# Optimization experiments

Measured on AMD Instinct MI355X. Metric: run time of the kernel, lower is better.

Reference implementation:

```python
import jax, jax.numpy as jnp
import numpy as np
import itertools

GRID_NUM = 12
VOXEL_SIZE = 0.12
OFFSET = GRID_NUM * VOXEL_SIZE / 2.0  # 0.72
G3 = GRID_NUM ** 3


def setup_inputs() -> dict:
    key = jax.random.key(0)
    k0, k1, k2, k3 = jax.random.split(key, 4)
    B, L0, L1, C = 4, 2048, 1024, 64
    x0 = jax.random.normal(k0, (B, L0, C), dtype=jnp.float32)
    x1 = jax.random.normal(k1, (B, L1, C), dtype=jnp.float32)
    # positions in [-0.3, 0.3) so delta_pos + OFFSET lies inside the grid [0, 1.44)
    pos0 = (jax.random.uniform(k2, (B, L0, 3), dtype=jnp.float32) - 0.5) * 0.6
    pos1 = (jax.random.uniform(k3, (B, L1, 3), dtype=jnp.float32) - 0.5) * 0.6
    return {"x0": x0, "x1": x1, "pos0": pos0, "pos1": pos1}


def _p2g_trilinear(pos, prob, seg, num_seg):
    """Trilinear point-to-grid splat.
    pos: (N,3) continuous coords in grid units' metric space; prob: (N,); seg: (N,) int segment id.
    Returns (num_seg, G3)."""
    c = pos / VOXEL_SIZE - 0.5          # voxel-center coordinates
    base = jnp.floor(c)
    frac = c - base                      # (N,3) in [0,1)
    base = base.astype(jnp.int32)
    out = jnp.zeros((num_seg * G3,), dtype=prob.dtype)
    for corner in itertools.product((0, 1), repeat=3):
        idx = base + jnp.asarray(corner, dtype=jnp.int32)  # (N,3)
        w = prob
        for d in range(3):
            w = w * (frac[:, d] if corner[d] else (1.0 - frac[:, d]))
        valid = jnp.all((idx >= 0) & (idx < GRID_NUM), axis=-1)
        flat = seg * G3 + idx[:, 0] * (GRID_NUM * GRID_NUM) + idx[:, 1] * GRID_NUM + idx[:, 2]
        flat = jnp.where(valid, flat, 0)
        out = out.at[flat].add(jnp.where(valid, w, 0.0))
    return out.reshape(num_seg, G3)


def reference(x0, x1, pos0, pos1):
    B, L0, C = x0.shape
    L1 = x1.shape[1]
    # scaled correlation + row softmax (stable; max-subtraction is math-identical)
    corr = jnp.einsum('blc,bmc->blm', x0, x1) / jnp.sqrt(jnp.asarray(C, x0.dtype))
    prob = jax.nn.softmax(corr, axis=-1)                       # (B,L0,L1)
    correspondence = jnp.einsum('blm,bmc->blc', prob, pos1)    # (B,L0,3)
    flow = correspondence - pos0
    # point-to-grid distribution of match probability over relative offsets
    delta = pos1[:, None, :, :] - pos0[:, :, None, :]          # (B,L0,L1,3)
    pos_f = delta.reshape(-1, 3) + OFFSET
    prob_f = prob.reshape(-1)
    N = B * L0 * L1
    seg = jnp.arange(N, dtype=jnp.int32) // L1                 # (N,) query-point segment id
    grid = _p2g_trilinear(pos_f, prob_f, seg, B * L0)          # (B*L0, G3)
    probs_grid = grid.reshape(B, L0, G3)
    return (flow, probs_grid)
```

## Files before the change

### kernel.cpp

```cpp
#include <hip/hip_runtime.h>
#include <stdint.h>

#define GRID_NUM 12
#define G3 1728
#define L0V 2048
#define L1V 1024
#define CV 64
#define RT 16

typedef __attribute__((ext_vector_type(8))) short short8;
typedef __attribute__((ext_vector_type(4))) short short4v;
typedef __attribute__((ext_vector_type(4))) float f32x4;

__device__ __forceinline__ unsigned short f2bf(float f) {
    union { float f; unsigned u; } v; v.f = f;
    unsigned u = v.u;
    u += 0x7fffu + ((u >> 16) & 1u);
    return (unsigned short)(u >> 16);
}
__device__ __forceinline__ float bf2f(unsigned short h) {
    union { unsigned u; float f; } v; v.u = ((unsigned)h) << 16;
    return v.f;
}

__device__ __forceinline__ void gload16(const void* g, void* l) {
    __builtin_amdgcn_global_load_lds(
        (const __attribute__((address_space(1))) unsigned int*)(uintptr_t)g,
        (__attribute__((address_space(3))) unsigned int*)(uintptr_t)l,
        16, 0, 0);
}

__global__ __launch_bounds__(256) void cvt_x1_kernel(
    const float* __restrict__ x1, unsigned short* __restrict__ ximg)
{
    const int g  = blockIdx.x * 256 + threadIdx.x;
    const int kg = g >> 3;
    const int j8 = g & 7;
    const int key = kg & 1023;
    const int ch  = key >> 6;
    const int kk  = key & 63;
    const int bi  = kg >> 10;

    const float4* src = (const float4*)(x1 + (size_t)kg * CV + j8 * 8);
    const float4 v0 = src[0], v1 = src[1];
    const float vv[8] = {v0.x, v0.y, v0.z, v0.w, v1.x, v1.y, v1.z, v1.w};
    short8 hi, lo;
    #pragma unroll
    for (int i = 0; i < 8; ++i) {
        const unsigned short h = f2bf(vv[i]);
        hi[i] = (short)h;
        lo[i] = (short)f2bf(vv[i] - bf2f(h));
    }
    char* base = (char*)ximg + ((size_t)(bi * 16 + ch)) * 16384;
    const int off = kk * 128 + ((j8 * 16) ^ ((kk & 7) << 4));
    *(short8*)(base + off) = hi;
    *(short8*)(base + 8192 + off) = lo;
}

__global__ __launch_bounds__(256) void cvt_pos_kernel(
    const float* __restrict__ pos1, float4* __restrict__ pos1p, int n)
{
    const int k = blockIdx.x * 256 + threadIdx.x;
    if (k < n) {
        float4 v;
        v.x = pos1[k * 3 + 0];
        v.y = pos1[k * 3 + 1];
        v.z = pos1[k * 3 + 2];
        v.w = 0.f;
        pos1p[k] = v;
    }
}

__global__ __launch_bounds__(256) void corr_probs_kernel(
    const float* __restrict__ x0, const unsigned short* __restrict__ ximg,
    const float* __restrict__ pos0, const float* __restrict__ pos1,
    float* __restrict__ out_flow, unsigned short* __restrict__ probs_bf,
    float* __restrict__ rscale)
{
    const int r0 = blockIdx.x * RT;
    const int b  = r0 >> 11;
    const int t  = threadIdx.x;
    const int lane = t & 63;
    const int w    = t >> 6;
    const int l15  = lane & 15;
    const int q    = lane >> 4;

    __shared__ __align__(16) short sX0h[RT * 64], sX0l[RT * 64];
    __shared__ __align__(16) char  sX1[2][16384];
    __shared__ __align__(16) float sp1[L1V * 3];
    __shared__ float sred[4][RT][4];

    {
        const int row = t >> 4;
        const float4 v = ((const float4*)(x0 + (size_t)(r0 + row) * CV))[t & 15];
        const unsigned short h0 = f2bf(v.x), h1 = f2bf(v.y), h2 = f2bf(v.z), h3 = f2bf(v.w);
        const short4v hi = { (short)h0, (short)h1, (short)h2, (short)h3 };
        const short4v lo = { (short)f2bf(v.x - bf2f(h0)), (short)f2bf(v.y - bf2f(h1)),
                             (short)f2bf(v.z - bf2f(h2)), (short)f2bf(v.w - bf2f(h3)) };
        const int off = row * 128 + (((t & 15) * 8) ^ ((row & 7) << 4));
        *(short4v*)((char*)sX0h + off) = hi;
        *(short4v*)((char*)sX0l + off) = lo;
    }
    {
        const float4* ps = (const float4*)(pos1 + (size_t)b * L1V * 3);
        #pragma unroll
        for (int i = 0; i < 3; ++i)
            ((float4*)sp1)[i * 256 + t] = ps[i * 256 + t];
    }

    const char* img = (const char*)ximg + (size_t)b * (16 * 16384);
    #pragma unroll
    for (int i = 0; i < 4; ++i)
        gload16(img + (w * 4 + i) * 1024 + lane * 16,
                sX1[0] + (w * 4 + i) * 1024);
    __syncthreads();

    const int ma    = w * 16 + l15;
    const int abase = ma * 128;
    const int asw   = (ma & 7) << 4;
    const int bbase = l15 * 128;
    const int bsw   = (l15 & 7) << 4;

    const int ka0 = (q * 8) * 2, ka1 = (32 + q * 8) * 2;
    const short8 bh0 = *(const short8*)((const char*)sX0h + bbase + (ka0 ^ bsw));
    const short8 bh1 = *(const short8*)((const char*)sX0h + bbase + (ka1 ^ bsw));
    const short8 bl0 = *(const short8*)((const char*)sX0l + bbase + (ka0 ^ bsw));
    const short8 bl1 = *(const short8*)((const char*)sX0l + bbase + (ka1 ^ bsw));

    float s_a = 0.f, cx_a = 0.f, cy_a = 0.f, cz_a = 0.f;

    for (int ch = 0; ch < 16; ++ch) {
        const int buf = ch & 1;
        if (ch < 15) {
            const char* s = img + (ch + 1) * 16384;
            char* d = sX1[buf ^ 1];
            #pragma unroll
            for (int i = 0; i < 4; ++i)
                gload16(s + (w * 4 + i) * 1024 + lane * 16, d + (w * 4 + i) * 1024);
            asm volatile("s_waitcnt vmcnt(4)" ::: "memory");
        } else {
            asm volatile("s_waitcnt vmcnt(1)" ::: "memory");
        }
        __builtin_amdgcn_s_barrier();

        const char* Xh = sX1[buf];
        const char* Xl = Xh + 8192;
        f32x4 acc = {0.f, 0.f, 0.f, 0.f};
        {
            const short8 ah0 = *(const short8*)(Xh + abase + (ka0 ^ asw));
            const short8 al0 = *(const short8*)(Xl + abase + (ka0 ^ asw));
            const short8 ah1 = *(const short8*)(Xh + abase + (ka1 ^ asw));
            const short8 al1 = *(const short8*)(Xl + abase + (ka1 ^ asw));
            acc = __builtin_amdgcn_mfma_f32_16x16x32_bf16(ah0, bh0, acc, 0, 0, 0);
            acc = __builtin_amdgcn_mfma_f32_16x16x32_bf16(ah0, bl0, acc, 0, 0, 0);
            acc = __builtin_amdgcn_mfma_f32_16x16x32_bf16(al0, bh0, acc, 0, 0, 0);
            acc = __builtin_amdgcn_mfma_f32_16x16x32_bf16(ah1, bh1, acc, 0, 0, 0);
            acc = __builtin_amdgcn_mfma_f32_16x16x32_bf16(ah1, bl1, acc, 0, 0, 0);
            acc = __builtin_amdgcn_mfma_f32_16x16x32_bf16(al1, bh1, acc, 0, 0, 0);
        }

        unsigned short eb[4];
        #pragma unroll
        for (int rg = 0; rg < 4; ++rg) {
            const int kc = ch * 64 + w * 16 + q * 4 + rg;
            const float e = __expf(acc[rg] * 0.125f);
            eb[rg] = f2bf(e);
            s_a += e;
            cx_a = fmaf(e, sp1[kc * 3 + 0], cx_a);
            cy_a = fmaf(e, sp1[kc * 3 + 1], cy_a);
            cz_a = fmaf(e, sp1[kc * 3 + 2], cz_a);
        }
        const short4v ev = { (short)eb[0], (short)eb[1], (short)eb[2], (short)eb[3] };
        *(short4v*)(probs_bf + (size_t)(r0 + l15) * L1V + ch * 64 + w * 16 + q * 4) = ev;

        __builtin_amdgcn_s_barrier();
    }

    s_a  += __shfl_xor(s_a, 16, 64);  s_a  += __shfl_xor(s_a, 32, 64);
    cx_a += __shfl_xor(cx_a, 16, 64); cx_a += __shfl_xor(cx_a, 32, 64);
    cy_a += __shfl_xor(cy_a, 16, 64); cy_a += __shfl_xor(cy_a, 32, 64);
    cz_a += __shfl_xor(cz_a, 16, 64); cz_a += __shfl_xor(cz_a, 32, 64);
    if (lane < 16) {
        sred[w][l15][0] = s_a;  sred[w][l15][1] = cx_a;
        sred[w][l15][2] = cy_a; sred[w][l15][3] = cz_a;
    }
    __syncthreads();

    if (t < RT) {
        const float S  = (sred[0][t][0] + sred[1][t][0]) + (sred[2][t][0] + sred[3][t][0]);
        const float CX = (sred[0][t][1] + sred[1][t][1]) + (sred[2][t][1] + sred[3][t][1]);
        const float CY = (sred[0][t][2] + sred[1][t][2]) + (sred[2][t][2] + sred[3][t][2]);
        const float CZ = (sred[0][t][3] + sred[1][t][3]) + (sred[2][t][3] + sred[3][t][3]);
        const float rs = 1.0f / S;
        rscale[r0 + t] = rs;
        out_flow[(r0 + t) * 3 + 0] = CX * rs - pos0[(r0 + t) * 3 + 0];
        out_flow[(r0 + t) * 3 + 1] = CY * rs - pos0[(r0 + t) * 3 + 1];
        out_flow[(r0 + t) * 3 + 2] = CZ * rs - pos0[(r0 + t) * 3 + 2];
    }
}

__global__ __launch_bounds__(256, 4) void splat_mfma_kernel(
    const unsigned short* __restrict__ probs_bf, const float* __restrict__ rscale,
    const float* __restrict__ pos0, const float4* __restrict__ pos1p,
    float* __restrict__ out_grid)
{
    const int t    = threadIdx.x;
    const int lane = t & 63;
    const int w    = t >> 6;
    const int r    = blockIdx.x * 4 + w;
    const int b    = r >> 11;

    __shared__ __align__(16) short sAll[4][4608];
    char* sR = (char*)sAll[w];
    char* sZ = (char*)sAll[w] + 8192;

    const float inv = 1.0f / 0.12f;
    const float p0x = pos0[r * 3 + 0];
    const float p0y = pos0[r * 3 + 1];
    const float p0z = pos0[r * 3 + 2];
    const float4* p1p = pos1p + (size_t)b * L1V;
    const unsigned short* prow = probs_bf + (size_t)r * L1V;

    const int mnx = (int)floorf((-0.3f - p0x + 0.72f) * inv - 0.5f);
    const int mny = (int)floorf((-0.3f - p0y + 0.72f) * inv - 0.5f);
    const int mnz = (int)floorf((-0.3f - p0z + 0.72f) * inv - 0.5f);

    {
        const short8 z8 = {0, 0, 0, 0, 0, 0, 0, 0};
        #pragma unroll
        for (int j = 0; j < 9; ++j)
            *(short8*)(sR + lane * 16 + j * 1024) = z8;
    }

    const int l15  = lane & 15;
    const int q16  = (lane >> 4) * 16;
    const int asw  = (l15 & 7) << 4;
    const int aoff0 = l15 * 128 + ((0  + q16) ^ asw);
    const int aoff1 = l15 * 128 + ((64 + q16) ^ asw);
    const int zrow = l15 & 7;
    const int bsw  = zrow << 4;
    const int boff0 = zrow * 128 + ((0  + q16) ^ bsw);
    const int boff1 = zrow * 128 + ((64 + q16) ^ bsw);
    const int lane2 = lane * 2;

    f32x4 acc[4];
    #pragma unroll
    for (int mt = 0; mt < 4; ++mt) acc[mt] = (f32x4){0.f, 0.f, 0.f, 0.f};

    char *P0 = sR + lane2, *P1 = sR + lane2, *P2 = sR + lane2,
         *P3 = sR + lane2, *P4 = sZ + lane2, *P5 = sZ + lane2;

    float4 pc = p1p[lane];
    float pv  = bf2f(prow[lane]);

    asm volatile("s_waitcnt lgkmcnt(0)" ::: "memory");

    for (int ch = 0; ch < 16; ++ch) {
        float4 nc = pc;
        float  nv = pv;
        if (ch < 15) {
            const int nk = (ch + 1) * 64 + lane;
            nc = p1p[nk];
            nv = bf2f(prow[nk]);
        }

        const float ax = ((pc.x - p0x) + 0.72f) * inv - 0.5f;
        const float ay = ((pc.y - p0y) + 0.72f) * inv - 0.5f;
        const float az = ((pc.z - p0z) + 0.72f) * inv - 0.5f;
        const float fxf = floorf(ax), fyf = floorf(ay), fzf = floorf(az);
        const float fx = ax - fxf, fy = ay - fyf, fz = az - fzf;
        const int rix = (int)fxf - mnx;
        const int riy = (int)fyf - mny;
        const int riz = (int)fzf - mnz;
        const float wx0 = 1.f - fx, wy0 = 1.f - fy, wz0 = 1.f - fz;
        const float a0p = pv * wx0, a1p = pv * fx;
        const unsigned short r00 = f2bf(a0p * wy0), r01 = f2bf(a0p * fy);
        const unsigned short r10 = f2bf(a1p * wy0), r11 = f2bf(a1p * fy);
        const unsigned short z0 = f2bf(wz0), z1 = f2bf(fz);

        const int c00 = rix * 8 + riy;
        char* A0 = sR + (c00    ) * 128 + (lane2 ^ (((c00    ) & 7) << 4));
        char* A1 = sR + (c00 + 1) * 128 + (lane2 ^ (((c00 + 1) & 7) << 4));
        char* A2 = sR + (c00 + 8) * 128 + (lane2 ^ (((c00 + 8) & 7) << 4));
        char* A3 = sR + (c00 + 9) * 128 + (lane2 ^ (((c00 + 9) & 7) << 4));
        char* Z0a = sZ + riz * 128 + (lane2 ^ (riz << 4));
        char* Z1a = sZ + (riz + 1) * 128 + (lane2 ^ ((riz + 1) << 4));

        *(short*)P0 = 0; *(short*)P1 = 0; *(short*)P2 = 0;
        *(short*)P3 = 0; *(short*)P4 = 0; *(short*)P5 = 0;
        *(short*)A0 = (short)r00; *(short*)A1 = (short)r01;
        *(short*)A2 = (short)r10; *(short*)A3 = (short)r11;
        *(short*)Z0a = (short)z0; *(short*)Z1a = (short)z1;

        const short8 b0 = *(const short8*)(sZ + boff0);
        const short8 b1 = *(const short8*)(sZ + boff1);
        #pragma unroll
        for (int mt = 0; mt < 4; ++mt) {
            const short8 a0 = *(const short8*)(sR + mt * 2048 + aoff0);
            const short8 a1 = *(const short8*)(sR + mt * 2048 + aoff1);
            acc[mt] = __builtin_amdgcn_mfma_f32_16x16x32_bf16(a0, b0, acc[mt], 0, 0, 0);
            acc[mt] = __builtin_amdgcn_mfma_f32_16x16x32_bf16(a1, b1, acc[mt], 0, 0, 0);
        }

        P0 = A0; P1 = A1; P2 = A2; P3 = A3; P4 = Z0a; P5 = Z1a;
        pc = nc; pv = nv;
    }

    const float rs = rscale[r];
    float* og = out_grid + (size_t)r * G3;
    {
        const float4 z4 = {0.f, 0.f, 0.f, 0.f};
        float4* og4 = (float4*)og;
        #pragma unroll
        for (int j = 0; j < 6; ++j) og4[j * 64 + lane] = z4;
        if (lane < 48) og4[384 + lane] = z4;
    }
    asm volatile("s_waitcnt vmcnt(0)" ::: "memory");

    const int zB = lane & 15;
    if (zB < 8) {
        const int gz = mnz + zB;
        if (gz <= 11) {
            const int h4 = (lane >> 4) * 4;
            const int rxm = 11 - mnx;
            const int rym = 11 - mny;
            float* base2 = og + mnx * 144 + mny * 12 + gz;
            #pragma unroll
            for (int mt = 0; mt < 4; ++mt) {
                #pragma unroll
                for (int rg = 0; rg < 4; ++rg) {
                    const int c  = mt * 16 + h4 + rg;
                    const int rx = c >> 3;
                    const int ry = c & 7;
                    if (rx <= rxm && ry <= rym)
                        base2[rx * 144 + ry * 12] = acc[mt][rg] * rs;
                }
            }
        }
    }
}

extern "C" void kernel_launch(void* const* d_in, const int* in_sizes, int n_in,
                              void* d_out, int out_size, void* d_ws, size_t ws_size,
                              hipStream_t stream) {
    const float* x0   = (const float*)d_in[0];
    const float* x1   = (const float*)d_in[1];
    const float* pos0 = (const float*)d_in[2];
    const float* pos1 = (const float*)d_in[3];
    float* out = (float*)d_out;

    const int B    = in_sizes[0] / (L0V * CV);
    const int rows = B * L0V;

    float* out_flow = out;
    float* out_grid = out + (size_t)rows * 3;

    unsigned short* probs_bf = (unsigned short*)d_ws;
    float* rscale = (float*)((char*)d_ws + (size_t)rows * L1V * sizeof(unsigned short));
    unsigned short* ximg = (unsigned short*)((char*)rscale + (size_t)rows * sizeof(float));
    float4* pos1p = (float4*)((char*)ximg + (size_t)B * 16 * 16384);

    const int nkeys = B * L1V;
    cvt_x1_kernel<<<(B * L1V * CV / 8) / 256, 256, 0, stream>>>(x1, ximg);
    cvt_pos_kernel<<<(nkeys + 255) / 256, 256, 0, stream>>>(pos1, pos1p, nkeys);
    corr_probs_kernel<<<rows / RT, 256, 0, stream>>>(
        x0, ximg, pos0, pos1, out_flow, probs_bf, rscale);
    splat_mfma_kernel<<<rows / 4, 256, 0, stream>>>(
        probs_bf, rscale, pos0, pos1p, out_grid);
}
```

Measured before the change: 62.35 us.

## Fuse correlation-softmax and grid splat into one kernel, keeping probs in LDS

Merges the correlation/exp kernel and the MFMA splat kernel into one kernel. Each block keeps its 16 rows of bf16 exp values in shared memory instead of writing them to global, then splats 4 rows per wave and computes the softmax sum and flow inside the splat loop. The two conversion kernels are also merged, cutting launch count and the global round-trip of the probability matrix. In exchange each block needs about 68 KB of LDS, so occupancy drops, and each wave now handles 4 rows serially, so splat parallelism per block falls.

```diff
diff --git a/kernel.cpp b/kernel.cpp
--- a/kernel.cpp
+++ b/kernel.cpp
@@ -30,8 +30,9 @@
         16, 0, 0);
 }
 
-__global__ __launch_bounds__(256) void cvt_x1_kernel(
-    const float* __restrict__ x1, unsigned short* __restrict__ ximg)
+__global__ __launch_bounds__(256) void cvt_kernel(
+    const float* __restrict__ x1, const float* __restrict__ pos1,
+    unsigned short* __restrict__ ximg, float4* __restrict__ pos1p, int nkeys)
 {
     const int g  = blockIdx.x * 256 + threadIdx.x;
     const int kg = g >> 3;
@@ -55,27 +56,21 @@
     const int off = kk * 128 + ((j8 * 16) ^ ((kk & 7) << 4));
     *(short8*)(base + off) = hi;
     *(short8*)(base + 8192 + off) = lo;
-}
-
-__global__ __launch_bounds__(256) void cvt_pos_kernel(
-    const float* __restrict__ pos1, float4* __restrict__ pos1p, int n)
-{
-    const int k = blockIdx.x * 256 + threadIdx.x;
-    if (k < n) {
+
+    if (g < nkeys) {
         float4 v;
-        v.x = pos1[k * 3 + 0];
-        v.y = pos1[k * 3 + 1];
-        v.z = pos1[k * 3 + 2];
+        v.x = pos1[g * 3 + 0];
+        v.y = pos1[g * 3 + 1];
+        v.z = pos1[g * 3 + 2];
         v.w = 0.f;
-        pos1p[k] = v;
-    }
-}
-
-__global__ __launch_bounds__(256) void corr_probs_kernel(
+        pos1p[g] = v;
+    }
+}
+
+__global__ __launch_bounds__(256) void fused_kernel(
     const float* __restrict__ x0, const unsigned short* __restrict__ ximg,
-    const float* __restrict__ pos0, const float* __restrict__ pos1,
-    float* __restrict__ out_flow, unsigned short* __restrict__ probs_bf,
-    float* __restrict__ rscale)
+    const float* __restrict__ pos0, const float4* __restrict__ pos1p,
+    float* __restrict__ out_flow, float* __restrict__ out_grid)
 {
     const int r0 = blockIdx.x * RT;
     const int b  = r0 >> 11;
@@ -85,10 +80,10 @@
     const int l15  = lane & 15;
     const int q    = lane >> 4;
 
-    __shared__ __align__(16) short sX0h[RT * 64], sX0l[RT * 64];
-    __shared__ __align__(16) char  sX1[2][16384];
-    __shared__ __align__(16) float sp1[L1V * 3];
-    __shared__ float sred[4][RT][4];
+    __shared__ __align__(16) char pool[69632];
+    char* sX0h = pool;
+    char* sX0l = pool + 2048;
+    char* sE   = pool + 36864;
 
     {
         const int row = t >> 4;
@@ -98,21 +93,15 @@
         const short4v lo = { (short)f2bf(v.x - bf2f(h0)), (short)f2bf(v.y - bf2f(h1)),
                              (short)f2bf(v.z - bf2f(h2)), (short)f2bf(v.w - bf2f(h3)) };
         const int off = row * 128 + (((t & 15) * 8) ^ ((row & 7) << 4));
-        *(short4v*)((char*)sX0h + off) = hi;
-        *(short4v*)((char*)sX0l + off) = lo;
-    }
-    {
-        const float4* ps = (const float4*)(pos1 + (size_t)b * L1V * 3);
-        #pragma unroll
-        for (int i = 0; i < 3; ++i)
-            ((float4*)sp1)[i * 256 + t] = ps[i * 256 + t];
+        *(short4v*)(sX0h + off) = hi;
+        *(short4v*)(sX0l + off) = lo;
     }
 
     const char* img = (const char*)ximg + (size_t)b * (16 * 16384);
     #pragma unroll
     for (int i = 0; i < 4; ++i)
         gload16(img + (w * 4 + i) * 1024 + lane * 16,
-                sX1[0] + (w * 4 + i) * 1024);
+                pool + 4096 + (w * 4 + i) * 1024);
     __syncthreads();
 
     const int ma    = w * 16 + l15;
@@ -120,30 +109,27 @@
     const int asw   = (ma & 7) << 4;
     const int bbase = l15 * 128;
     const int bsw   = (l15 & 7) << 4;
-
     const int ka0 = (q * 8) * 2, ka1 = (32 + q * 8) * 2;
-    const short8 bh0 = *(const short8*)((const char*)sX0h + bbase + (ka0 ^ bsw));
-    const short8 bh1 = *(const short8*)((const char*)sX0h + bbase + (ka1 ^ bsw));
-    const short8 bl0 = *(const short8*)((const char*)sX0l + bbase + (ka0 ^ bsw));
-    const short8 bl1 = *(const short8*)((const char*)sX0l + bbase + (ka1 ^ bsw));
-
-    float s_a = 0.f, cx_a = 0.f, cy_a = 0.f, cz_a = 0.f;
+    const short8 bh0 = *(const short8*)(sX0h + bbase + (ka0 ^ bsw));
+    const short8 bh1 = *(const short8*)(sX0h + bbase + (ka1 ^ bsw));
+    const short8 bl0 = *(const short8*)(sX0l + bbase + (ka0 ^ bsw));
+    const short8 bl1 = *(const short8*)(sX0l + bbase + (ka1 ^ bsw));
 
     for (int ch = 0; ch < 16; ++ch) {
         const int buf = ch & 1;
         if (ch < 15) {
             const char* s = img + (ch + 1) * 16384;
-            char* d = sX1[buf ^ 1];
+            char* d = pool + 4096 + (buf ^ 1) * 16384;
             #pragma unroll
             for (int i = 0; i < 4; ++i)
                 gload16(s + (w * 4 + i) * 1024 + lane * 16, d + (w * 4 + i) * 1024);
             asm volatile("s_waitcnt vmcnt(4)" ::: "memory");
         } else {
-            asm volatile("s_waitcnt vmcnt(1)" ::: "memory");
+            asm volatile("s_waitcnt vmcnt(0)" ::: "memory");
         }
         __builtin_amdgcn_s_barrier();
 
-        const char* Xh = sX1[buf];
+        const char* Xh = pool + 4096 + buf * 16384;
         const char* Xl = Xh + 8192;
         f32x4 acc = {0.f, 0.f, 0.f, 0.f};
         {
@@ -161,69 +147,20 @@
 
         unsigned short eb[4];
         #pragma unroll
-        for (int rg = 0; rg < 4; ++rg) {
-            const int kc = ch * 64 + w * 16 + q * 4 + rg;
-            const float e = __expf(acc[rg] * 0.125f);
-            eb[rg] = f2bf(e);
-            s_a += e;
-            cx_a = fmaf(e, sp1[kc * 3 + 0], cx_a);
-            cy_a = fmaf(e, sp1[kc * 3 + 1], cy_a);
-            cz_a = fmaf(e, sp1[kc * 3 + 2], cz_a);
-        }
+        for (int rg = 0; rg < 4; ++rg)
+            eb[rg] = f2bf(__expf(acc[rg] * 0.125f));
         const short4v ev = { (short)eb[0], (short)eb[1], (short)eb[2], (short)eb[3] };
-        *(short4v*)(probs_bf + (size_t)(r0 + l15) * L1V + ch * 64 + w * 16 + q * 4) = ev;
+        const int col = (ch * 64 + w * 16 + q * 4) ^ (l15 << 2);
+        *(short4v*)(sE + l15 * 2048 + col * 2) = ev;
 
         __builtin_amdgcn_s_barrier();
     }
-
-    s_a  += __shfl_xor(s_a, 16, 64);  s_a  += __shfl_xor(s_a, 32, 64);
-    cx_a += __shfl_xor(cx_a, 16, 64); cx_a += __shfl_xor(cx_a, 32, 64);
-    cy_a += __shfl_xor(cy_a, 16, 64); cy_a += __shfl_xor(cy_a, 32, 64);
-    cz_a += __shfl_xor(cz_a, 16, 64); cz_a += __shfl_xor(cz_a, 32, 64);
-    if (lane < 16) {
-        sred[w][l15][0] = s_a;  sred[w][l15][1] = cx_a;
-        sred[w][l15][2] = cy_a; sred[w][l15][3] = cz_a;
-    }
     __syncthreads();
 
-    if (t < RT) {
-        const float S  = (sred[0][t][0] + sred[1][t][0]) + (sred[2][t][0] + sred[3][t][0]);
-        const float CX = (sred[0][t][1] + sred[1][t][1]) + (sred[2][t][1] + sred[3][t][1]);
-        const float CY = (sred[0][t][2] + sred[1][t][2]) + (sred[2][t][2] + sred[3][t][2]);
-        const float CZ = (sred[0][t][3] + sred[1][t][3]) + (sred[2][t][3] + sred[3][t][3]);
-        const float rs = 1.0f / S;
-        rscale[r0 + t] = rs;
-        out_flow[(r0 + t) * 3 + 0] = CX * rs - pos0[(r0 + t) * 3 + 0];
-        out_flow[(r0 + t) * 3 + 1] = CY * rs - pos0[(r0 + t) * 3 + 1];
-        out_flow[(r0 + t) * 3 + 2] = CZ * rs - pos0[(r0 + t) * 3 + 2];
-    }
-}
-
-__global__ __launch_bounds__(256, 4) void splat_mfma_kernel(
-    const unsigned short* __restrict__ probs_bf, const float* __restrict__ rscale,
-    const float* __restrict__ pos0, const float4* __restrict__ pos1p,
-    float* __restrict__ out_grid)
-{
-    const int t    = threadIdx.x;
-    const int lane = t & 63;
-    const int w    = t >> 6;
-    const int r    = blockIdx.x * 4 + w;
-    const int b    = r >> 11;
-
-    __shared__ __align__(16) short sAll[4][4608];
-    char* sR = (char*)sAll[w];
-    char* sZ = (char*)sAll[w] + 8192;
-
+    char* sR = pool + w * 9216;
+    char* sZ = sR + 8192;
     const float inv = 1.0f / 0.12f;
-    const float p0x = pos0[r * 3 + 0];
-    const float p0y = pos0[r * 3 + 1];
-    const float p0z = pos0[r * 3 + 2];
     const float4* p1p = pos1p + (size_t)b * L1V;
-    const unsigned short* prow = probs_bf + (size_t)r * L1V;
-
-    const int mnx = (int)floorf((-0.3f - p0x + 0.72f) * inv - 0.5f);
-    const int mny = (int)floorf((-0.3f - p0y + 0.72f) * inv - 0.5f);
-    const int mnz = (int)floorf((-0.3f - p0z + 0.72f) * inv - 0.5f);
 
     {
         const short8 z8 = {0, 0, 0, 0, 0, 0, 0, 0};
@@ -232,108 +169,139 @@
             *(short8*)(sR + lane * 16 + j * 1024) = z8;
     }
 
-    const int l15  = lane & 15;
     const int q16  = (lane >> 4) * 16;
-    const int asw  = (l15 & 7) << 4;
-    const int aoff0 = l15 * 128 + ((0  + q16) ^ asw);
-    const int aoff1 = l15 * 128 + ((64 + q16) ^ asw);
+    const int asw2 = (l15 & 7) << 4;
+    const int aoff0 = l15 * 128 + ((0  + q16) ^ asw2);
+    const int aoff1 = l15 * 128 + ((64 + q16) ^ asw2);
     const int zrow = l15 & 7;
-    const int bsw  = zrow << 4;
-    const int boff0 = zrow * 128 + ((0  + q16) ^ bsw);
-    const int boff1 = zrow * 128 + ((64 + q16) ^ bsw);
+    const int bsw2 = zrow << 4;
+    const int boff0 = zrow * 128 + ((0  + q16) ^ bsw2);
+    const int boff1 = zrow * 128 + ((64 + q16) ^ bsw2);
     const int lane2 = lane * 2;
 
-    f32x4 acc[4];
-    #pragma unroll
-    for (int mt = 0; mt < 4; ++mt) acc[mt] = (f32x4){0.f, 0.f, 0.f, 0.f};
-
-    char *P0 = sR + lane2, *P1 = sR + lane2, *P2 = sR + lane2,
-         *P3 = sR + lane2, *P4 = sZ + lane2, *P5 = sZ + lane2;
-
-    float4 pc = p1p[lane];
-    float pv  = bf2f(prow[lane]);
-
-    asm volatile("s_waitcnt lgkmcnt(0)" ::: "memory");
-
-    for (int ch = 0; ch < 16; ++ch) {
-        float4 nc = pc;
-        float  nv = pv;
-        if (ch < 15) {
-            const int nk = (ch + 1) * 64 + lane;
-            nc = p1p[nk];
-            nv = bf2f(prow[nk]);
-        }
-
-        const float ax = ((pc.x - p0x) + 0.72f) * inv - 0.5f;
-        const float ay = ((pc.y - p0y) + 0.72f) * inv - 0.5f;
-        const float az = ((pc.z - p0z) + 0.72f) * inv - 0.5f;
-        const float fxf = floorf(ax), fyf = floorf(ay), fzf = floorf(az);
-        const float fx = ax - fxf, fy = ay - fyf, fz = az - fzf;
-        const int rix = (int)fxf - mnx;
-        const int riy = (int)fyf - mny;
-        const int riz = (int)fzf - mnz;
-        const float wx0 = 1.f - fx, wy0 = 1.f - fy, wz0 = 1.f - fz;
-        const float a0p = pv * wx0, a1p = pv * fx;
-        const unsigned short r00 = f2bf(a0p * wy0), r01 = f2bf(a0p * fy);
-        const unsigned short r10 = f2bf(a1p * wy0), r11 = f2bf(a1p * fy);
-        const unsigned short z0 = f2bf(wz0), z1 = f2bf(fz);
-
-        const int c00 = rix * 8 + riy;
-        char* A0 = sR + (c00    ) * 128 + (lane2 ^ (((c00    ) & 7) << 4));
-        char* A1 = sR + (c00 + 1) * 128 + (lane2 ^ (((c00 + 1) & 7) << 4));
-        char* A2 = sR + (c00 + 8) * 128 + (lane2 ^ (((c00 + 8) & 7) << 4));
-        char* A3 = sR + (c00 + 9) * 128 + (lane2 ^ (((c00 + 9) & 7) << 4));
-        char* Z0a = sZ + riz * 128 + (lane2 ^ (riz << 4));
-        char* Z1a = sZ + (riz + 1) * 128 + (lane2 ^ ((riz + 1) << 4));
+    for (int rr4 = 0; rr4 < 4; ++rr4) {
+        const int rrow = w * 4 + rr4;
+        const int r    = r0 + rrow;
+        const float p0x = pos0[r * 3 + 0];
+        const float p0y = pos0[r * 3 + 1];
+        const float p0z = pos0[r * 3 + 2];
+        const int mnx = (int)floorf((-0.3f - p0x + 0.72f) * inv - 0.5f);
+        const int mny = (int)floorf((-0.3f - p0y + 0.72f) * inv - 0.5f);
+        const int mnz = (int)floorf((-0.3f - p0z + 0.72f) * inv - 0.5f);
+        const int esw = rrow << 2;
+
+        f32x4 acc[4];
+        #pragma unroll
+        for (int mt = 0; mt < 4; ++mt) acc[mt] = (f32x4){0.f, 0.f, 0.f, 0.f};
+        float s_a = 0.f, cx_a = 0.f, cy_a = 0.f, cz_a = 0.f;
+
+        char *P0 = sR + lane2, *P1 = sR + lane2, *P2 = sR + lane2,
+             *P3 = sR + lane2, *P4 = sZ + lane2, *P5 = sZ + lane2;
+
+        float4 pc = p1p[lane];
+        float  pv = bf2f(*(const unsigned short*)(sE + rrow * 2048 + (lane ^ esw) * 2));
+
+        for (int ch = 0; ch < 16; ++ch) {
+            float4 nc = pc;
+            float  nv = pv;
+            if (ch < 15) {
+                const int nk = (ch + 1) * 64 + lane;
+                nc = p1p[nk];
+                nv = bf2f(*(const unsigned short*)(sE + rrow * 2048 + (nk ^ esw) * 2));
+            }
+
+            s_a += pv;
+            cx_a = fmaf(pv, pc.x, cx_a);
+            cy_a = fmaf(pv, pc.y, cy_a);
+            cz_a = fmaf(pv, pc.z, cz_a);
+
+            const float ax = ((pc.x - p0x) + 0.72f) * inv - 0.5f;
+            const float ay = ((pc.y - p0y) + 0.72f) * inv - 0.5f;
+            const float az = ((pc.z - p0z) + 0.72f) * inv - 0.5f;
+            const float fxf = floorf(ax), fyf = floorf(ay), fzf = floorf(az);
+            const float fx = ax - fxf, fy = ay - fyf, fz = az - fzf;
+            const int rix = (int)fxf - mnx;
+            const int riy = (int)fyf - mny;
+            const int riz = (int)fzf - mnz;
+            const float wx0 = 1.f - fx, wy0 = 1.f - fy, wz0 = 1.f - fz;
+            const float a0p = pv * wx0, a1p = pv * fx;
+            const unsigned short r00 = f2bf(a0p * wy0), r01 = f2bf(a0p * fy);
+            const unsigned short r10 = f2bf(a1p * wy0), r11 = f2bf(a1p * fy);
+            const unsigned short z0 = f2bf(wz0), z1 = f2bf(fz);
+
+            const int c00 = rix * 8 + riy;
+            char* A0 = sR + (c00    ) * 128 + (lane2 ^ (((c00    ) & 7) << 4));
+            char* A1 = sR + (c00 + 1) * 128 + (lane2 ^ (((c00 + 1) & 7) << 4));
+            char* A2 = sR + (c00 + 8) * 128 + (lane2 ^ (((c00 + 8) & 7) << 4));
+            char* A3 = sR + (c00 + 9) * 128 + (lane2 ^ (((c00 + 9) & 7) << 4));
+            char* Z0a = sZ + riz * 128 + (lane2 ^ (riz << 4));
+            char* Z1a = sZ + (riz + 1) * 128 + (lane2 ^ ((riz + 1) << 4));
+
+            *(short*)P0 = 0; *(short*)P1 = 0; *(short*)P2 = 0;
+            *(short*)P3 = 0; *(short*)P4 = 0; *(short*)P5 = 0;
+            *(short*)A0 = (short)r00; *(short*)A1 = (short)r01;
+            *(short*)A2 = (short)r10; *(short*)A3 = (short)r11;
+            *(short*)Z0a = (short)z0; *(short*)Z1a = (short)z1;
+
+            const short8 b0 = *(const short8*)(sZ + boff0);
+            const short8 b1 = *(const short8*)(sZ + boff1);
+            #pragma unroll
+            for (int mt = 0; mt < 4; ++mt) {
+                const short8 a0 = *(const short8*)(sR + mt * 2048 + aoff0);
+                const short8 a1 = *(const short8*)(sR + mt * 2048 + aoff1);
+                acc[mt] = __builtin_amdgcn_mfma_f32_16x16x32_bf16(a0, b0, acc[mt], 0, 0, 0);
+                acc[mt] = __builtin_amdgcn_mfma_f32_16x16x32_bf16(a1, b1, acc[mt], 0, 0, 0);
+            }
+
+            P0 = A0; P1 = A1; P2 = A2; P3 = A3; P4 = Z0a; P5 = Z1a;
+            pc = nc; pv = nv;
+        }
 
         *(short*)P0 = 0; *(short*)P1 = 0; *(short*)P2 = 0;
         *(short*)P3 = 0; *(short*)P4 = 0; *(short*)P5 = 0;
-        *(short*)A0 = (short)r00; *(short*)A1 = (short)r01;
-        *(short*)A2 = (short)r10; *(short*)A3 = (short)r11;
-        *(short*)Z0a = (short)z0; *(short*)Z1a = (short)z1;
-
-        const short8 b0 = *(const short8*)(sZ + boff0);
-        const short8 b1 = *(const short8*)(sZ + boff1);
+
         #pragma unroll
-        for (int mt = 0; mt < 4; ++mt) {
-            const short8 a0 = *(const short8*)(sR + mt * 2048 + aoff0);
-            const short8 a1 = *(const short8*)(sR + mt * 2048 + aoff1);
-            acc[mt] = __builtin_amdgcn_mfma_f32_16x16x32_bf16(a0, b0, acc[mt], 0, 0, 0);
-            acc[mt] = __builtin_amdgcn_mfma_f32_16x16x32_bf16(a1, b1, acc[mt], 0, 0, 0);
-        }
-
-        P0 = A0; P1 = A1; P2 = A2; P3 = A3; P4 = Z0a; P5 = Z1a;
-        pc = nc; pv = nv;
-    }
-
-    const float rs = rscale[r];
-    float* og = out_grid + (size_t)r * G3;
-    {
-        const float4 z4 = {0.f, 0.f, 0.f, 0.f};
-        float4* og4 = (float4*)og;
-        #pragma unroll
-        for (int j = 0; j < 6; ++j) og4[j * 64 + lane] = z4;
-        if (lane < 48) og4[384 + lane] = z4;
-    }
-    asm volatile("s_waitcnt vmcnt(0)" ::: "memory");
-
-    const int zB = lane & 15;
-    if (zB < 8) {
-        const int gz = mnz + zB;
-        if (gz <= 11) {
-            const int h4 = (lane >> 4) * 4;
-            const int rxm = 11 - mnx;
-            const int rym = 11 - mny;
-            float* base2 = og + mnx * 144 + mny * 12 + gz;
+        for (int o = 1; o < 64; o <<= 1) {
+            s_a  += __shfl_xor(s_a, o, 64);
+            cx_a += __shfl_xor(cx_a, o, 64);
+            cy_a += __shfl_xor(cy_a, o, 64);
+            cz_a += __shfl_xor(cz_a, o, 64);
+        }
+        const float rs = 1.0f / s_a;
+        if (lane == 0) {
+            out_flow[r * 3 + 0] = cx_a * rs - p0x;
+            out_flow[r * 3 + 1] = cy_a * rs - p0y;
+            out_flow[r * 3 + 2] = cz_a * rs - p0z;
+        }
+
+        float* og = out_grid + (size_t)r * G3;
+        {
+            const float4 z4 = {0.f, 0.f, 0.f, 0.f};
+            float4* og4 = (float4*)og;
             #pragma unroll
-            for (int mt = 0; mt < 4; ++mt) {
+            for (int j = 0; j < 6; ++j) og4[j * 64 + lane] = z4;
+            if (lane < 48) og4[384 + lane] = z4;
+        }
+        asm volatile("s_waitcnt vmcnt(0)" ::: "memory");
+
+        const int zB = lane & 15;
+        if (zB < 8) {
+            const int gz = mnz + zB;
+            if (gz <= 11) {
+                const int h4 = (lane >> 4) * 4;
+                const int rxm = 11 - mnx;
+                const int rym = 11 - mny;
+                float* base2 = og + mnx * 144 + mny * 12 + gz;
                 #pragma unroll
-                for (int rg = 0; rg < 4; ++rg) {
-                    const int c  = mt * 16 + h4 + rg;
-                    const int rx = c >> 3;
-                    const int ry = c & 7;
-                    if (rx <= rxm && ry <= rym)
-                        base2[rx * 144 + ry * 12] = acc[mt][rg] * rs;
+                for (int mt = 0; mt < 4; ++mt) {
+                    #pragma unroll
+                    for (int rg = 0; rg < 4; ++rg) {
+                        const int c  = mt * 16 + h4 + rg;
+                        const int rx = c >> 3;
+                        const int ry = c & 7;
+                        if (rx <= rxm && ry <= rym)
+                            base2[rx * 144 + ry * 12] = acc[mt][rg] * rs;
+                    }
                 }
             }
         }
@@ -355,16 +323,12 @@
     float* out_flow = out;
     float* out_grid = out + (size_t)rows * 3;
 
-    unsigned short* probs_bf = (unsigned short*)d_ws;
-    float* rscale = (float*)((char*)d_ws + (size_t)rows * L1V * sizeof(unsigned short));
-    unsigned short* ximg = (unsigned short*)((char*)rscale + (size_t)rows * sizeof(float));
-    float4* pos1p = (float4*)((char*)ximg + (size_t)B * 16 * 16384);
+    unsigned short* ximg = (unsigned short*)d_ws;
+    float4* pos1p = (float4*)((char*)d_ws + (size_t)B * 16 * 16384);
 
     const int nkeys = B * L1V;
-    cvt_x1_kernel<<<(B * L1V * CV / 8) / 256, 256, 0, stream>>>(x1, ximg);
-    cvt_pos_kernel<<<(nkeys + 255) / 256, 256, 0, stream>>>(pos1, pos1p, nkeys);
-    corr_probs_kernel<<<rows / RT, 256, 0, stream>>>(
-        x0, ximg, pos0, pos1, out_flow, probs_bf, rscale);
-    splat_mfma_kernel<<<rows / 4, 256, 0, stream>>>(
-        probs_bf, rscale, pos0, pos1p, out_grid);
-}
+    cvt_kernel<<<(B * L1V * CV / 8) / 256, 256, 0, stream>>>(
+        x1, pos1, ximg, pos1p, nkeys);
+    fused_kernel<<<rows / RT, 256, 0, stream>>>(
+        x0, ximg, pos0, pos1p, out_flow, out_grid);
+}
```

Result: faster. 60.04 us (-3.7%).

## Drop x1 low-bf16 split, merge conversion kernels, remove per-chunk barriers

Applied to the files above, without the earlier changes.

Each x1 value is now stored as a single bf16 instead of a hi/lo split. This halves the LDS image and the per-chunk global-to-LDS traffic, and cuts MFMAs per chunk from six to four. The two preprocessing kernels are merged into one launch. The workgroup barriers in the correlation loop become scheduling barriers, since each wave only reads the LDS rows it loaded itself. The splat kernel's grid-coordinate computation is folded into a single FMA. The trade-off is lower correlation accuracy before the exponential, which could push outputs toward the tolerance limit.

```diff
diff --git a/kernel.cpp b/kernel.cpp
--- a/kernel.cpp
+++ b/kernel.cpp
@@ -30,8 +30,9 @@
         16, 0, 0);
 }
 
-__global__ __launch_bounds__(256) void cvt_x1_kernel(
-    const float* __restrict__ x1, unsigned short* __restrict__ ximg)
+__global__ __launch_bounds__(256) void cvt_kernel(
+    const float* __restrict__ x1, const float* __restrict__ pos1,
+    unsigned short* __restrict__ ximg, float4* __restrict__ pos1p, int nkeys)
 {
     const int g  = blockIdx.x * 256 + threadIdx.x;
     const int kg = g >> 3;
@@ -43,31 +44,22 @@
 
     const float4* src = (const float4*)(x1 + (size_t)kg * CV + j8 * 8);
     const float4 v0 = src[0], v1 = src[1];
-    const float vv[8] = {v0.x, v0.y, v0.z, v0.w, v1.x, v1.y, v1.z, v1.w};
-    short8 hi, lo;
-    #pragma unroll
-    for (int i = 0; i < 8; ++i) {
-        const unsigned short h = f2bf(vv[i]);
-        hi[i] = (short)h;
-        lo[i] = (short)f2bf(vv[i] - bf2f(h));
-    }
-    char* base = (char*)ximg + ((size_t)(bi * 16 + ch)) * 16384;
+    short8 hi;
+    hi[0] = (short)f2bf(v0.x); hi[1] = (short)f2bf(v0.y);
+    hi[2] = (short)f2bf(v0.z); hi[3] = (short)f2bf(v0.w);
+    hi[4] = (short)f2bf(v1.x); hi[5] = (short)f2bf(v1.y);
+    hi[6] = (short)f2bf(v1.z); hi[7] = (short)f2bf(v1.w);
+    char* base = (char*)ximg + ((size_t)(bi * 16 + ch)) * 8192;
     const int off = kk * 128 + ((j8 * 16) ^ ((kk & 7) << 4));
     *(short8*)(base + off) = hi;
-    *(short8*)(base + 8192 + off) = lo;
-}
-
-__global__ __launch_bounds__(256) void cvt_pos_kernel(
-    const float* __restrict__ pos1, float4* __restrict__ pos1p, int n)
-{
-    const int k = blockIdx.x * 256 + threadIdx.x;
-    if (k < n) {
+
+    if (g < nkeys) {
         float4 v;
-        v.x = pos1[k * 3 + 0];
-        v.y = pos1[k * 3 + 1];
-        v.z = pos1[k * 3 + 2];
+        v.x = pos1[g * 3 + 0];
+        v.y = pos1[g * 3 + 1];
+        v.z = pos1[g * 3 + 2];
         v.w = 0.f;
-        pos1p[k] = v;
+        pos1p[g] = v;
     }
 }
 
@@ -86,7 +78,7 @@
     const int q    = lane >> 4;
 
     __shared__ __align__(16) short sX0h[RT * 64], sX0l[RT * 64];
-    __shared__ __align__(16) char  sX1[2][16384];
+    __shared__ __align__(16) char  sX1[2][8192];
     __shared__ __align__(16) float sp1[L1V * 3];
     __shared__ float sred[4][RT][4];
 
@@ -108,11 +100,11 @@
             ((float4*)sp1)[i * 256 + t] = ps[i * 256 + t];
     }
 
-    const char* img = (const char*)ximg + (size_t)b * (16 * 16384);
+    const char* img = (const char*)ximg + (size_t)b * (16 * 8192);
     #pragma unroll
-    for (int i = 0; i < 4; ++i)
-        gload16(img + (w * 4 + i) * 1024 + lane * 16,
-                sX1[0] + (w * 4 + i) * 1024);
+    for (int i = 0; i < 2; ++i)
+        gload16(img + (w * 2 + i) * 1024 + lane * 16,
+                sX1[0] + (w * 2 + i) * 1024);
     __syncthreads();
 
     const int ma    = w * 16 + l15;
@@ -120,7 +112,6 @@
     const int asw   = (ma & 7) << 4;
     const int bbase = l15 * 128;
     const int bsw   = (l15 & 7) << 4;
-
     const int ka0 = (q * 8) * 2, ka1 = (32 + q * 8) * 2;
     const short8 bh0 = *(const short8*)((const char*)sX0h + bbase + (ka0 ^ bsw));
     const short8 bh1 = *(const short8*)((const char*)sX0h + bbase + (ka1 ^ bsw));
@@ -131,32 +122,28 @@
 
     for (int ch = 0; ch < 16; ++ch) {
         const int buf = ch & 1;
+        __builtin_amdgcn_sched_barrier(0);
         if (ch < 15) {
-            const char* s = img + (ch + 1) * 16384;
+            const char* s = img + (ch + 1) * 8192;
             char* d = sX1[buf ^ 1];
             #pragma unroll
-            for (int i = 0; i < 4; ++i)
-                gload16(s + (w * 4 + i) * 1024 + lane * 16, d + (w * 4 + i) * 1024);
-            asm volatile("s_waitcnt vmcnt(4)" ::: "memory");
+            for (int i = 0; i < 2; ++i)
+                gload16(s + (w * 2 + i) * 1024 + lane * 16, d + (w * 2 + i) * 1024);
+            asm volatile("s_waitcnt vmcnt(2)" ::: "memory");
         } else {
-            asm volatile("s_waitcnt vmcnt(1)" ::: "memory");
-        }
-        __builtin_amdgcn_s_barrier();
+            asm volatile("s_waitcnt vmcnt(0)" ::: "memory");
+        }
+        __builtin_amdgcn_sched_barrier(0);
 
         const char* Xh = sX1[buf];
-        const char* Xl = Xh + 8192;
         f32x4 acc = {0.f, 0.f, 0.f, 0.f};
         {
             const short8 ah0 = *(const short8*)(Xh + abase + (ka0 ^ asw));
-            const short8 al0 = *(const short8*)(Xl + abase + (ka0 ^ asw));
             const short8 ah1 = *(const short8*)(Xh + abase + (ka1 ^ asw));
-            const short8 al1 = *(const short8*)(Xl + abase + (ka1 ^ asw));
             acc = __builtin_amdgcn_mfma_f32_16x16x32_bf16(ah0, bh0, acc, 0, 0, 0);
             acc = __builtin_amdgcn_mfma_f32_16x16x32_bf16(ah0, bl0, acc, 0, 0, 0);
-            acc = __builtin_amdgcn_mfma_f32_16x16x32_bf16(al0, bh0, acc, 0, 0, 0);
             acc = __builtin_amdgcn_mfma_f32_16x16x32_bf16(ah1, bh1, acc, 0, 0, 0);
             acc = __builtin_amdgcn_mfma_f32_16x16x32_bf16(ah1, bl1, acc, 0, 0, 0);
-            acc = __builtin_amdgcn_mfma_f32_16x16x32_bf16(al1, bh1, acc, 0, 0, 0);
         }
 
         unsigned short eb[4];
@@ -172,8 +159,6 @@
         }
         const short4v ev = { (short)eb[0], (short)eb[1], (short)eb[2], (short)eb[3] };
         *(short4v*)(probs_bf + (size_t)(r0 + l15) * L1V + ch * 64 + w * 16 + q * 4) = ev;
-
-        __builtin_amdgcn_s_barrier();
     }
 
     s_a  += __shfl_xor(s_a, 16, 64);  s_a  += __shfl_xor(s_a, 32, 64);
@@ -221,9 +206,12 @@
     const float4* p1p = pos1p + (size_t)b * L1V;
     const unsigned short* prow = probs_bf + (size_t)r * L1V;
 
-    const int mnx = (int)floorf((-0.3f - p0x + 0.72f) * inv - 0.5f);
-    const int mny = (int)floorf((-0.3f - p0y + 0.72f) * inv - 0.5f);
-    const int mnz = (int)floorf((-0.3f - p0z + 0.72f) * inv - 0.5f);
+    const float kx = (0.72f - p0x) * inv - 0.5f;
+    const float ky = (0.72f - p0y) * inv - 0.5f;
+    const float kz = (0.72f - p0z) * inv - 0.5f;
+    const int mnx = (int)floorf(-0.3f * inv + kx);
+    const int mny = (int)floorf(-0.3f * inv + ky);
+    const int mnz = (int)floorf(-0.3f * inv + kz);
 
     {
         const short8 z8 = {0, 0, 0, 0, 0, 0, 0, 0};
@@ -234,13 +222,13 @@
 
     const int l15  = lane & 15;
     const int q16  = (lane >> 4) * 16;
-    const int asw  = (l15 & 7) << 4;
-    const int aoff0 = l15 * 128 + ((0  + q16) ^ asw);
-    const int aoff1 = l15 * 128 + ((64 + q16) ^ asw);
+    const int asw2 = (l15 & 7) << 4;
+    const int aoff0 = l15 * 128 + ((0  + q16) ^ asw2);
+    const int aoff1 = l15 * 128 + ((64 + q16) ^ asw2);
     const int zrow = l15 & 7;
-    const int bsw  = zrow << 4;
-    const int boff0 = zrow * 128 + ((0  + q16) ^ bsw);
-    const int boff1 = zrow * 128 + ((64 + q16) ^ bsw);
+    const int bsw2 = zrow << 4;
+    const int boff0 = zrow * 128 + ((0  + q16) ^ bsw2);
+    const int boff1 = zrow * 128 + ((64 + q16) ^ bsw2);
     const int lane2 = lane * 2;
 
     f32x4 acc[4];
@@ -251,7 +239,7 @@
          *P3 = sR + lane2, *P4 = sZ + lane2, *P5 = sZ + lane2;
 
     float4 pc = p1p[lane];
-    float pv  = bf2f(prow[lane]);
+    float  pv = bf2f(prow[lane]);
 
     asm volatile("s_waitcnt lgkmcnt(0)" ::: "memory");
 
@@ -264,9 +252,9 @@
             nv = bf2f(prow[nk]);
         }
 
-        const float ax = ((pc.x - p0x) + 0.72f) * inv - 0.5f;
-        const float ay = ((pc.y - p0y) + 0.72f) * inv - 0.5f;
-        const float az = ((pc.z - p0z) + 0.72f) * inv - 0.5f;
+        const float ax = fmaf(pc.x, inv, kx);
+        const float ay = fmaf(pc.y, inv, ky);
+        const float az = fmaf(pc.z, inv, kz);
         const float fxf = floorf(ax), fyf = floorf(ay), fzf = floorf(az);
         const float fx = ax - fxf, fy = ay - fyf, fz = az - fzf;
         const int rix = (int)fxf - mnx;
@@ -358,11 +346,11 @@
     unsigned short* probs_bf = (unsigned short*)d_ws;
     float* rscale = (float*)((char*)d_ws + (size_t)rows * L1V * sizeof(unsigned short));
     unsigned short* ximg = (unsigned short*)((char*)rscale + (size_t)rows * sizeof(float));
-    float4* pos1p = (float4*)((char*)ximg + (size_t)B * 16 * 16384);
+    float4* pos1p = (float4*)((char*)ximg + (size_t)B * 16 * 8192);
 
     const int nkeys = B * L1V;
-    cvt_x1_kernel<<<(B * L1V * CV / 8) / 256, 256, 0, stream>>>(x1, ximg);
-    cvt_pos_kernel<<<(nkeys + 255) / 256, 256, 0, stream>>>(pos1, pos1p, nkeys);
+    cvt_kernel<<<(B * L1V * CV / 8) / 256, 256, 0, stream>>>(
+        x1, pos1, ximg, pos1p, nkeys);
     corr_probs_kernel<<<rows / RT, 256, 0, stream>>>(
         x0, ximg, pos0, pos1, out_flow, probs_bf, rscale);
     splat_mfma_kernel<<<rows / 4, 256, 0, stream>>>(
```

Result: faster. 57.90 us (-7.1%).
